# Optimization experiments

Measured on AMD Instinct MI355X. Metric: run time of the kernel, lower is better.

The kernel has to match this reference:

```python
import jax, jax.numpy as jnp
import numpy as np

B, T, F, H = 1024, 512, 16, 64


def setup_inputs() -> dict:
    key = jax.random.key(0)
    ks = jax.random.split(key, 8)
    return {
        "x": jax.random.normal(ks[0], (B, T, F), jnp.float32),
        "W": jax.random.normal(ks[1], (F, 3 * H), jnp.float32) * 0.1,
        "U": jax.random.normal(ks[2], (H, 3 * H), jnp.float32) * 0.1,
        "b": jax.random.normal(ks[3], (2, 3 * H), jnp.float32) * 0.1,
        "w1": jax.random.normal(ks[4], (H, 64), jnp.float32) * 0.1,
        "b1": jax.random.normal(ks[5], (64,), jnp.float32) * 0.1,
        "gamma": jnp.ones((64,), jnp.float32),
        "beta": jnp.zeros((64,), jnp.float32),
        "mov_mean": jnp.zeros((64,), jnp.float32),
        "mov_var": jnp.ones((64,), jnp.float32),
        "w2": jax.random.normal(ks[6], (64, 1), jnp.float32) * 0.1,
        "b2": jax.random.normal(ks[7], (1,), jnp.float32) * 0.1,
    }


def _gru_last(x, W, U, b):
    # Keras GRU, reset_after=True, inference (no dropout). Returns last hidden state [B,H].
    b_i, b_r = b[0], b[1]
    xp = jnp.einsum("btf,fg->btg", x, W) + b_i  # [B,T,3H] precomputed input projections
    xp_t = jnp.transpose(xp, (1, 0, 2))          # [T,B,3H]
    h0 = jnp.zeros((x.shape[0], H), x.dtype)

    def step(h, xpt):
        rec = h @ U + b_r                         # [B,3H]
        xz, xr, xh = jnp.split(xpt, 3, axis=-1)
        rz, rr, rh = jnp.split(rec, 3, axis=-1)
        z = jax.nn.sigmoid(xz + rz)
        r = jax.nn.sigmoid(xr + rr)
        hh = jnp.tanh(xh + r * rh)
        h_new = z * h + (1.0 - z) * hh
        return h_new, None

    h_last, _ = jax.lax.scan(step, h0, xp_t)
    return h_last


def reference(x, W, U, b, w1, b1, gamma, beta, mov_mean, mov_var, w2, b2):
    h = _gru_last(x, W, U, b)                     # [B,H]
    y = jax.nn.relu(h @ w1 + b1)                  # Dense(64, relu)
    # Dropout: identity in inference. BatchNorm: inference with moving stats.
    eps = 1e-3  # Keras BatchNormalization default epsilon
    y = (y - mov_mean) * jax.lax.rsqrt(mov_var + eps) * gamma + beta
    out = y @ w2 + b2                             # [B,1]
    return out
```

## Files before the change

### kernel.cpp

```cpp
#include <hip/hip_runtime.h>
#include <hip/hip_fp16.h>


#define T_ 512
#define F_ 16
#define H_ 64

typedef _Float16 half_t;
typedef _Float16 h2 __attribute__((ext_vector_type(2)));
typedef _Float16 h4 __attribute__((ext_vector_type(4)));
typedef _Float16 h8 __attribute__((ext_vector_type(8)));

__device__ __forceinline__ float fdot2f(h2 a, h2 b, float c) {
#if __has_builtin(__builtin_amdgcn_fdot2)
    return __builtin_amdgcn_fdot2(a, b, c, false);
#else
    return fmaf((float)a.x, (float)b.x, fmaf((float)a.y, (float)b.y, c));
#endif
}

__device__ __forceinline__ float fast_rcp(float a) {
    return __builtin_amdgcn_rcpf(a);
}
__device__ __forceinline__ float sigm(float a) {
    return fast_rcp(1.0f + __expf(-a));
}
__device__ __forceinline__ float tanh_fast(float a) {
    return 1.0f - 2.0f * fast_rcp(__expf(2.0f * a) + 1.0f);
}

__global__ __launch_bounds__(64, 1) void gru_fused(
    const float* __restrict__ x, const float* __restrict__ W,
    const float* __restrict__ U, const float* __restrict__ b,
    const float* __restrict__ w1, const float* __restrict__ b1,
    const float* __restrict__ gamma_, const float* __restrict__ beta_,
    const float* __restrict__ mmean, const float* __restrict__ mvar,
    const float* __restrict__ w2, const float* __restrict__ b2,
    float* __restrict__ out)
{
    __shared__ __align__(16) half_t xs16[T_ * F_];
    __shared__ __align__(16) half_t hb16[H_];

    const int j   = threadIdx.x;
    const int row = blockIdx.x;

    const float4* xr4 = (const float4*)(x + (size_t)row * (T_ * F_));
    #pragma unroll
    for (int i = 0; i < (T_ * F_ / 4) / 64; ++i) {
        const float4 v = xr4[i * 64 + j];
        h4 p = { (half_t)v.x, (half_t)v.y, (half_t)v.z, (half_t)v.w };
        ((h4*)xs16)[i * 64 + j] = p;
    }
    hb16[j] = (half_t)0.0f;

    h2 uz2[32], ur2[32], uh2[32];
    #pragma unroll
    for (int m = 0; m < 32; ++m) {
        uz2[m] = h2{ (half_t)U[(2*m)*192 +       j], (half_t)U[(2*m+1)*192 +       j] };
        ur2[m] = h2{ (half_t)U[(2*m)*192 +  64 + j], (half_t)U[(2*m+1)*192 +  64 + j] };
        uh2[m] = h2{ (half_t)U[(2*m)*192 + 128 + j], (half_t)U[(2*m+1)*192 + 128 + j] };
    }
    h2 wz2[8], wr2[8], wh2[8];
    #pragma unroll
    for (int p = 0; p < 8; ++p) {
        wz2[p] = h2{ (half_t)W[(2*p)*192 +       j], (half_t)W[(2*p+1)*192 +       j] };
        wr2[p] = h2{ (half_t)W[(2*p)*192 +  64 + j], (half_t)W[(2*p+1)*192 +  64 + j] };
        wh2[p] = h2{ (half_t)W[(2*p)*192 + 128 + j], (half_t)W[(2*p+1)*192 + 128 + j] };
    }
    const float bz  = b[j]       + b[192 + j];
    const float brr = b[64 + j]  + b[256 + j];
    const float bxh = b[128 + j];
    const float brh = b[320 + j];

    __syncthreads();

    float h = 0.0f;
    for (int t = 0; t < T_; ++t) {
        h2 xp[8];
        #pragma unroll
        for (int q = 0; q < 2; ++q)
            *((h8*)&xp[4 * q]) = ((const h8*)xs16)[t * 2 + q];
        h2 hp[32];
        #pragma unroll
        for (int q = 0; q < 8; ++q)
            *((h8*)&hp[4 * q]) = ((const h8*)hb16)[q];

        float az = bz, ar = brr, axh = bxh, arh = brh;

        #pragma unroll
        for (int p = 0; p < 8; ++p) {
            az  = fdot2f(xp[p], wz2[p], az);
            ar  = fdot2f(xp[p], wr2[p], ar);
            axh = fdot2f(xp[p], wh2[p], axh);
        }
        #pragma unroll
        for (int m = 0; m < 32; ++m) {
            az  = fdot2f(hp[m], uz2[m], az);
            ar  = fdot2f(hp[m], ur2[m], ar);
            arh = fdot2f(hp[m], uh2[m], arh);
        }

        const float z  = sigm(az);
        const float r  = sigm(ar);
        const float hh = tanh_fast(fmaf(r, arh, axh));
        h = fmaf(z, h - hh, hh);

        hb16[j] = (half_t)h;
    }

    float y = b1[j];
    const int hb2 = __float_as_int(h);
    #pragma unroll
    for (int k = 0; k < H_; ++k) {
        const float hk = __int_as_float(__builtin_amdgcn_readlane(hb2, k));
        y = fmaf(hk, w1[k * H_ + j], y);
    }
    y = fmaxf(y, 0.0f);
    y = fmaf((y - mmean[j]) * rsqrtf(mvar[j] + 1e-3f), gamma_[j], beta_[j]);

    float acc = y * w2[j];
    #pragma unroll
    for (int off = 32; off > 0; off >>= 1)
        acc += __shfl_down(acc, off, 64);
    if (j == 0) out[row] = acc + b2[0];
}

extern "C" void kernel_launch(void* const* d_in, const int* in_sizes, int n_in,
                              void* d_out, int out_size, void* d_ws, size_t ws_size,
                              hipStream_t stream) {
    const float* x      = (const float*)d_in[0];
    const float* W      = (const float*)d_in[1];
    const float* U      = (const float*)d_in[2];
    const float* b      = (const float*)d_in[3];
    const float* w1     = (const float*)d_in[4];
    const float* b1     = (const float*)d_in[5];
    const float* gamma_ = (const float*)d_in[6];
    const float* beta_  = (const float*)d_in[7];
    const float* mmean  = (const float*)d_in[8];
    const float* mvar   = (const float*)d_in[9];
    const float* w2     = (const float*)d_in[10];
    const float* b2     = (const float*)d_in[11];
    float* out = (float*)d_out;

    const int B = in_sizes[0] / (T_ * F_);
    gru_fused<<<B, 64, 0, stream>>>(x, W, U, b, w1, b1, gamma_, beta_,
                                    mmean, mvar, w2, b2, out);
}
```

Before: 264.7 us.

## Split GRU recurrent reduction across two wavefronts with shared-memory combine

Each batch row now uses two wavefronts instead of one. Each wave computes half of the hidden and input dot products, and the partial sums are exchanged through a double-buffered shared-memory area with one barrier per timestep. Both waves then apply the gate nonlinearities redundantly and keep their own copy of the hidden state. The per-step dot products are also split into two independent accumulator chains. The aim is to shorten the serial per-step latency and double the number of waves per CU, at the cost of a block-wide barrier and extra LDS traffic every step.

```diff
diff --git a/kernel.cpp b/kernel.cpp
--- a/kernel.cpp
+++ b/kernel.cpp
@@ -29,7 +29,7 @@
     return 1.0f - 2.0f * fast_rcp(__expf(2.0f * a) + 1.0f);
 }
 
-__global__ __launch_bounds__(64, 1) void gru_fused(
+__global__ __launch_bounds__(128, 2) void gru_fused(
     const float* __restrict__ x, const float* __restrict__ W,
     const float* __restrict__ U, const float* __restrict__ b,
     const float* __restrict__ w1, const float* __restrict__ b1,
@@ -39,73 +39,91 @@
     float* __restrict__ out)
 {
     __shared__ __align__(16) half_t xs16[T_ * F_];
-    __shared__ __align__(16) half_t hb16[H_];
+    __shared__ __align__(16) half_t hbw[2][H_];
+    __shared__ __align__(16) float  comb[2 * 2 * 64 * 4];
 
-    const int j   = threadIdx.x;
+    const int tid = threadIdx.x;
+    const int j   = tid & 63;
+    const int w   = tid >> 6;
     const int row = blockIdx.x;
 
     const float4* xr4 = (const float4*)(x + (size_t)row * (T_ * F_));
     #pragma unroll
-    for (int i = 0; i < (T_ * F_ / 4) / 64; ++i) {
-        const float4 v = xr4[i * 64 + j];
+    for (int i = 0; i < (T_ * F_ / 4) / 128; ++i) {
+        const float4 v = xr4[i * 128 + tid];
         h4 p = { (half_t)v.x, (half_t)v.y, (half_t)v.z, (half_t)v.w };
-        ((h4*)xs16)[i * 64 + j] = p;
+        ((h4*)xs16)[i * 128 + tid] = p;
     }
-    hb16[j] = (half_t)0.0f;
+    hbw[w][j] = (half_t)0.0f;
 
-    h2 uz2[32], ur2[32], uh2[32];
+    const int k0 = w * 32;
+    h2 uz2[16], ur2[16], uh2[16];
     #pragma unroll
-    for (int m = 0; m < 32; ++m) {
-        uz2[m] = h2{ (half_t)U[(2*m)*192 +       j], (half_t)U[(2*m+1)*192 +       j] };
-        ur2[m] = h2{ (half_t)U[(2*m)*192 +  64 + j], (half_t)U[(2*m+1)*192 +  64 + j] };
-        uh2[m] = h2{ (half_t)U[(2*m)*192 + 128 + j], (half_t)U[(2*m+1)*192 + 128 + j] };
+    for (int m = 0; m < 16; ++m) {
+        const int k = k0 + 2 * m;
+        uz2[m] = h2{ (half_t)U[k * 192 +       j], (half_t)U[(k + 1) * 192 +       j] };
+        ur2[m] = h2{ (half_t)U[k * 192 +  64 + j], (half_t)U[(k + 1) * 192 +  64 + j] };
+        uh2[m] = h2{ (half_t)U[k * 192 + 128 + j], (half_t)U[(k + 1) * 192 + 128 + j] };
     }
-    h2 wz2[8], wr2[8], wh2[8];
+    const int f0 = w * 8;
+    h2 wz2[4], wr2[4], wh2[4];
     #pragma unroll
-    for (int p = 0; p < 8; ++p) {
-        wz2[p] = h2{ (half_t)W[(2*p)*192 +       j], (half_t)W[(2*p+1)*192 +       j] };
-        wr2[p] = h2{ (half_t)W[(2*p)*192 +  64 + j], (half_t)W[(2*p+1)*192 +  64 + j] };
-        wh2[p] = h2{ (half_t)W[(2*p)*192 + 128 + j], (half_t)W[(2*p+1)*192 + 128 + j] };
+    for (int p = 0; p < 4; ++p) {
+        const int f = f0 + 2 * p;
+        wz2[p] = h2{ (half_t)W[f * 192 +       j], (half_t)W[(f + 1) * 192 +       j] };
+        wr2[p] = h2{ (half_t)W[f * 192 +  64 + j], (half_t)W[(f + 1) * 192 +  64 + j] };
+        wh2[p] = h2{ (half_t)W[f * 192 + 128 + j], (half_t)W[(f + 1) * 192 + 128 + j] };
     }
-    const float bz  = b[j]       + b[192 + j];
-    const float brr = b[64 + j]  + b[256 + j];
-    const float bxh = b[128 + j];
-    const float brh = b[320 + j];
+    float bz = 0.f, brr = 0.f, bxh = 0.f, brh = 0.f;
+    if (w == 0) {
+        bz  = b[j]      + b[192 + j];
+        brr = b[64 + j] + b[256 + j];
+        bxh = b[128 + j];
+        brh = b[320 + j];
+    }
 
     __syncthreads();
 
     float h = 0.0f;
     for (int t = 0; t < T_; ++t) {
-        h2 xp[8];
+        h2 hp[16];
         #pragma unroll
-        for (int q = 0; q < 2; ++q)
-            *((h8*)&xp[4 * q]) = ((const h8*)xs16)[t * 2 + q];
-        h2 hp[32];
-        #pragma unroll
-        for (int q = 0; q < 8; ++q)
-            *((h8*)&hp[4 * q]) = ((const h8*)hb16)[q];
+        for (int q = 0; q < 4; ++q)
+            *((h8*)&hp[4 * q]) = ((const h8*)&hbw[w][k0])[q];
+        h2 xp[4];
+        *((h8*)&xp[0]) = *((const h8*)&xs16[t * F_ + f0]);
 
-        float az = bz, ar = brr, axh = bxh, arh = brh;
+        float az0 = bz, ar0 = brr, axh = bxh, arh0 = brh;
+        float az1 = 0.f, ar1 = 0.f, arh1 = 0.f;
 
         #pragma unroll
-        for (int p = 0; p < 8; ++p) {
-            az  = fdot2f(xp[p], wz2[p], az);
-            ar  = fdot2f(xp[p], wr2[p], ar);
+        for (int p = 0; p < 4; ++p) {
+            az0 = fdot2f(xp[p], wz2[p], az0);
+            ar0 = fdot2f(xp[p], wr2[p], ar0);
             axh = fdot2f(xp[p], wh2[p], axh);
         }
         #pragma unroll
-        for (int m = 0; m < 32; ++m) {
-            az  = fdot2f(hp[m], uz2[m], az);
-            ar  = fdot2f(hp[m], ur2[m], ar);
-            arh = fdot2f(hp[m], uh2[m], arh);
+        for (int m = 0; m < 16; m += 2) {
+            az0  = fdot2f(hp[m],     uz2[m],     az0);
+            ar0  = fdot2f(hp[m],     ur2[m],     ar0);
+            arh0 = fdot2f(hp[m],     uh2[m],     arh0);
+            az1  = fdot2f(hp[m + 1], uz2[m + 1], az1);
+            ar1  = fdot2f(hp[m + 1], ur2[m + 1], ar1);
+            arh1 = fdot2f(hp[m + 1], uh2[m + 1], arh1);
         }
 
-        const float z  = sigm(az);
-        const float r  = sigm(ar);
-        const float hh = tanh_fast(fmaf(r, arh, axh));
+        const int par = t & 1;
+        *(float4*)&comb[((par * 2 + w) * 64 + j) * 4] =
+            make_float4(az0 + az1, ar0 + ar1, axh, arh0 + arh1);
+        __syncthreads();
+        const float4 o = *(const float4*)&comb[((par * 2 + (1 - w)) * 64 + j) * 4];
+
+        const float z  = sigm(az0 + az1 + o.x);
+        const float r  = sigm(ar0 + ar1 + o.y);
+        const float hh = tanh_fast(fmaf(r, arh0 + arh1 + o.w, axh + o.z));
         h = fmaf(z, h - hh, hh);
 
-        hb16[j] = (half_t)h;
+        hbw[w][j] = (half_t)h;
     }
 
     float y = b1[j];
@@ -122,7 +140,7 @@
     #pragma unroll
     for (int off = 32; off > 0; off >>= 1)
         acc += __shfl_down(acc, off, 64);
-    if (j == 0) out[row] = acc + b2[0];
+    if (tid == 0) out[row] = acc + b2[0];
 }
 
 extern "C" void kernel_launch(void* const* d_in, const int* in_sizes, int n_in,
@@ -143,6 +161,6 @@
     float* out = (float*)d_out;
 
     const int B = in_sizes[0] / (T_ * F_);
-    gru_fused<<<B, 64, 0, stream>>>(x, W, U, b, w1, b1, gamma_, beta_,
-                                    mmean, mvar, w2, b2, out);
+    gru_fused<<<B, 128, 0, stream>>>(x, W, U, b, w1, b1, gamma_, beta_,
+                                     mmean, mvar, w2, b2, out);
 }
```

Result: slower. 343.8 us (+29.9%).

## Batch 16 rows per block and compute GRU gates with MFMA

Applied to the files above, without the earlier changes.

Each 256-thread block now processes 16 batch rows, computing the gate projections for input and hidden state with 16x16x32 f16 MFMA instructions instead of per-thread fdot2 loops. The hidden state is double-buffered in shared memory with one barrier per timestep, and x is prefetched one step ahead from global memory instead of being staged in LDS. The head MLP is adapted to produce four rows per wave. This trades per-thread scalar dot-product work for matrix-core throughput but cuts the grid to B/16 blocks, lowering parallelism across CUs and adding a block-wide sync per step.

```diff
diff --git a/kernel.cpp b/kernel.cpp
--- a/kernel.cpp
+++ b/kernel.cpp
@@ -5,19 +5,12 @@
 #define T_ 512
 #define F_ 16
 #define H_ 64
+#define ROWS_ 16
+#define HSS 80
 
 typedef _Float16 half_t;
-typedef _Float16 h2 __attribute__((ext_vector_type(2)));
-typedef _Float16 h4 __attribute__((ext_vector_type(4)));
 typedef _Float16 h8 __attribute__((ext_vector_type(8)));
-
-__device__ __forceinline__ float fdot2f(h2 a, h2 b, float c) {
-#if __has_builtin(__builtin_amdgcn_fdot2)
-    return __builtin_amdgcn_fdot2(a, b, c, false);
-#else
-    return fmaf((float)a.x, (float)b.x, fmaf((float)a.y, (float)b.y, c));
-#endif
-}
+typedef float f32x4 __attribute__((ext_vector_type(4)));
 
 __device__ __forceinline__ float fast_rcp(float a) {
     return __builtin_amdgcn_rcpf(a);
@@ -29,7 +22,7 @@
     return 1.0f - 2.0f * fast_rcp(__expf(2.0f * a) + 1.0f);
 }
 
-__global__ __launch_bounds__(64, 1) void gru_fused(
+__global__ __launch_bounds__(256, 1) void gru_fused(
     const float* __restrict__ x, const float* __restrict__ W,
     const float* __restrict__ U, const float* __restrict__ b,
     const float* __restrict__ w1, const float* __restrict__ b1,
@@ -38,91 +31,126 @@
     const float* __restrict__ w2, const float* __restrict__ b2,
     float* __restrict__ out)
 {
-    __shared__ __align__(16) half_t xs16[T_ * F_];
-    __shared__ __align__(16) half_t hb16[H_];
+    __shared__ __align__(16) half_t hs[2][ROWS_][HSS];
+    __shared__ float hf[ROWS_][H_ + 4];
 
-    const int j   = threadIdx.x;
-    const int row = blockIdx.x;
+    const int tid = threadIdx.x;
+    const int w   = tid >> 6;
+    const int l   = tid & 63;
+    const int c   = l & 15;
+    const int q   = l >> 4;
+    const int r0  = blockIdx.x * ROWS_;
+    const int col = 16 * w + c;
 
-    const float4* xr4 = (const float4*)(x + (size_t)row * (T_ * F_));
+    for (int i = tid; i < 2 * ROWS_ * HSS; i += 256)
+        ((half_t*)hs)[i] = (half_t)0.0f;
+
+    h8 buz[2], bur[2], buh[2];
     #pragma unroll
-    for (int i = 0; i < (T_ * F_ / 4) / 64; ++i) {
-        const float4 v = xr4[i * 64 + j];
-        h4 p = { (half_t)v.x, (half_t)v.y, (half_t)v.z, (half_t)v.w };
-        ((h4*)xs16)[i * 64 + j] = p;
+    for (int cc = 0; cc < 2; ++cc) {
+        #pragma unroll
+        for (int i = 0; i < 8; ++i) {
+            const int k = 32 * cc + 8 * q + i;
+            buz[cc][i] = (half_t)U[k * 192 +       col];
+            bur[cc][i] = (half_t)U[k * 192 +  64 + col];
+            buh[cc][i] = (half_t)U[k * 192 + 128 + col];
+        }
     }
-    hb16[j] = (half_t)0.0f;
-
-    h2 uz2[32], ur2[32], uh2[32];
+    h8 bwz, bwr, bwh;
     #pragma unroll
-    for (int m = 0; m < 32; ++m) {
-        uz2[m] = h2{ (half_t)U[(2*m)*192 +       j], (half_t)U[(2*m+1)*192 +       j] };
-        ur2[m] = h2{ (half_t)U[(2*m)*192 +  64 + j], (half_t)U[(2*m+1)*192 +  64 + j] };
-        uh2[m] = h2{ (half_t)U[(2*m)*192 + 128 + j], (half_t)U[(2*m+1)*192 + 128 + j] };
+    for (int i = 0; i < 8; ++i) {
+        const int k = 8 * q + i;
+        const bool real = (q < 2);
+        bwz[i] = real ? (half_t)W[k * 192 +       col] : (half_t)0.0f;
+        bwr[i] = real ? (half_t)W[k * 192 +  64 + col] : (half_t)0.0f;
+        bwh[i] = real ? (half_t)W[k * 192 + 128 + col] : (half_t)0.0f;
     }
-    h2 wz2[8], wr2[8], wh2[8];
-    #pragma unroll
-    for (int p = 0; p < 8; ++p) {
-        wz2[p] = h2{ (half_t)W[(2*p)*192 +       j], (half_t)W[(2*p+1)*192 +       j] };
-        wr2[p] = h2{ (half_t)W[(2*p)*192 +  64 + j], (half_t)W[(2*p+1)*192 +  64 + j] };
-        wh2[p] = h2{ (half_t)W[(2*p)*192 + 128 + j], (half_t)W[(2*p+1)*192 + 128 + j] };
-    }
-    const float bz  = b[j]       + b[192 + j];
-    const float brr = b[64 + j]  + b[256 + j];
-    const float bxh = b[128 + j];
-    const float brh = b[320 + j];
+    const float bz  = b[col]       + b[192 + col];
+    const float br_ = b[64 + col]  + b[256 + col];
+    const float bxh = b[128 + col];
+    const float brh = b[320 + col];
 
     __syncthreads();
 
-    float h = 0.0f;
+    float hold[4] = {0.f, 0.f, 0.f, 0.f};
+
+    const float* xrow = x + (size_t)(r0 + c) * (T_ * F_) + 8 * (q & 1);
+    float4 xfa = *(const float4*)(xrow);
+    float4 xfb = *(const float4*)(xrow + 4);
+
     for (int t = 0; t < T_; ++t) {
-        h2 xp[8];
+        const int nb = t & 1;
+
+        h8 ax;
+        ax[0] = (half_t)xfa.x; ax[1] = (half_t)xfa.y;
+        ax[2] = (half_t)xfa.z; ax[3] = (half_t)xfa.w;
+        ax[4] = (half_t)xfb.x; ax[5] = (half_t)xfb.y;
+        ax[6] = (half_t)xfb.z; ax[7] = (half_t)xfb.w;
+
+        const int tn = (t + 1 < T_) ? (t + 1) : t;
+        const float4 nxa = *(const float4*)(xrow + tn * F_);
+        const float4 nxb = *(const float4*)(xrow + tn * F_ + 4);
+
+        const half_t* hrow = &hs[nb][c][0];
+        const h8 ah0 = *(const h8*)(hrow + 8 * q);
+        const h8 ah1 = *(const h8*)(hrow + 32 + 8 * q);
+
+        f32x4 cz  = {bz,  bz,  bz,  bz };
+        f32x4 cr  = {br_, br_, br_, br_};
+        f32x4 crh = {brh, brh, brh, brh};
+        f32x4 cxh = {bxh, bxh, bxh, bxh};
+        cz  = __builtin_amdgcn_mfma_f32_16x16x32_f16(ax,  bwz,    cz,  0, 0, 0);
+        cr  = __builtin_amdgcn_mfma_f32_16x16x32_f16(ax,  bwr,    cr,  0, 0, 0);
+        cxh = __builtin_amdgcn_mfma_f32_16x16x32_f16(ax,  bwh,    cxh, 0, 0, 0);
+        cz  = __builtin_amdgcn_mfma_f32_16x16x32_f16(ah0, buz[0], cz,  0, 0, 0);
+        cr  = __builtin_amdgcn_mfma_f32_16x16x32_f16(ah0, bur[0], cr,  0, 0, 0);
+        crh = __builtin_amdgcn_mfma_f32_16x16x32_f16(ah0, buh[0], crh, 0, 0, 0);
+        cz  = __builtin_amdgcn_mfma_f32_16x16x32_f16(ah1, buz[1], cz,  0, 0, 0);
+        cr  = __builtin_amdgcn_mfma_f32_16x16x32_f16(ah1, bur[1], cr,  0, 0, 0);
+        crh = __builtin_amdgcn_mfma_f32_16x16x32_f16(ah1, buh[1], crh, 0, 0, 0);
+
+        half_t* wrp = &hs[nb ^ 1][0][0] + col;
         #pragma unroll
-        for (int q = 0; q < 2; ++q)
-            *((h8*)&xp[4 * q]) = ((const h8*)xs16)[t * 2 + q];
-        h2 hp[32];
-        #pragma unroll
-        for (int q = 0; q < 8; ++q)
-            *((h8*)&hp[4 * q]) = ((const h8*)hb16)[q];
-
-        float az = bz, ar = brr, axh = bxh, arh = brh;
-
-        #pragma unroll
-        for (int p = 0; p < 8; ++p) {
-            az  = fdot2f(xp[p], wz2[p], az);
-            ar  = fdot2f(xp[p], wr2[p], ar);
-            axh = fdot2f(xp[p], wh2[p], axh);
-        }
-        #pragma unroll
-        for (int m = 0; m < 32; ++m) {
-            az  = fdot2f(hp[m], uz2[m], az);
-            ar  = fdot2f(hp[m], ur2[m], ar);
-            arh = fdot2f(hp[m], uh2[m], arh);
+        for (int i = 0; i < 4; ++i) {
+            const float z  = sigm(cz[i]);
+            const float r  = sigm(cr[i]);
+            const float hh = tanh_fast(fmaf(r, crh[i], cxh[i]));
+            hold[i] = fmaf(z, hold[i] - hh, hh);
+            wrp[(4 * q + i) * HSS] = (half_t)hold[i];
         }
 
-        const float z  = sigm(az);
-        const float r  = sigm(ar);
-        const float hh = tanh_fast(fmaf(r, arh, axh));
-        h = fmaf(z, h - hh, hh);
-
-        hb16[j] = (half_t)h;
+        xfa = nxa; xfb = nxb;
+        __syncthreads();
     }
 
-    float y = b1[j];
-    const int hb2 = __float_as_int(h);
     #pragma unroll
+    for (int i = 0; i < 4; ++i)
+        hf[4 * q + i][col] = hold[i];
+    __syncthreads();
+
+    const int j = l;
+    float y0 = b1[j], y1 = y0, y2 = y0, y3 = y0;
+    #pragma unroll 8
     for (int k = 0; k < H_; ++k) {
-        const float hk = __int_as_float(__builtin_amdgcn_readlane(hb2, k));
-        y = fmaf(hk, w1[k * H_ + j], y);
+        const float wk = w1[k * 64 + j];
+        y0 = fmaf(hf[4 * w + 0][k], wk, y0);
+        y1 = fmaf(hf[4 * w + 1][k], wk, y1);
+        y2 = fmaf(hf[4 * w + 2][k], wk, y2);
+        y3 = fmaf(hf[4 * w + 3][k], wk, y3);
     }
-    y = fmaxf(y, 0.0f);
-    y = fmaf((y - mmean[j]) * rsqrtf(mvar[j] + 1e-3f), gamma_[j], beta_[j]);
-
-    float acc = y * w2[j];
+    const float sc = rsqrtf(mvar[j] + 1e-3f) * gamma_[j];
+    const float mm = mmean[j], bt = beta_[j], v2 = w2[j];
+    float yy[4] = {y0, y1, y2, y3};
     #pragma unroll
-    for (int off = 32; off > 0; off >>= 1)
-        acc += __shfl_down(acc, off, 64);
-    if (j == 0) out[row] = acc + b2[0];
+    for (int ri = 0; ri < 4; ++ri) {
+        float yv = fmaxf(yy[ri], 0.0f);
+        yv = (yv - mm) * sc + bt;
+        float acc = yv * v2;
+        #pragma unroll
+        for (int off = 32; off > 0; off >>= 1)
+            acc += __shfl_down(acc, off, 64);
+        if (l == 0) out[r0 + 4 * w + ri] = acc + b2[0];
+    }
 }
 
 extern "C" void kernel_launch(void* const* d_in, const int* in_sizes, int n_in,
@@ -143,6 +171,6 @@
     float* out = (float*)d_out;
 
     const int B = in_sizes[0] / (T_ * F_);
-    gru_fused<<<B, 64, 0, stream>>>(x, W, U, b, w1, b1, gamma_, beta_,
-                                    mmean, mvar, w2, b2, out);
+    gru_fused<<<B / ROWS_, 256, 0, stream>>>(x, W, U, b, w1, b1, gamma_, beta_,
+                                             mmean, mvar, w2, b2, out);
 }
```

Result: slower. 304.8 us (+15.2%).
